# Optimization experiments

Hardware: AMD Instinct MI355X
Metric: run time of the kernel (lower is better)

The kernel has to match this reference:

```python
import jax, jax.numpy as jnp
import numpy as np

B, S, D, H = 4, 2048, 1024, 16
DK = D // H


def setup_inputs() -> dict:
    key = jax.random.key(0)
    ks = jax.random.split(key, 12)
    std = 0.02
    inp = {
        "query": jax.random.normal(ks[0], (B, S, D), jnp.float32),
        "key": jax.random.normal(ks[1], (B, S, D), jnp.float32),
        "value": jax.random.normal(ks[2], (B, S, D), jnp.float32),
        "mask": jnp.ones((B, 1, 1, S), jnp.int32),
        "Wq": jax.random.normal(ks[3], (D, D), jnp.float32) * std,
        "bq": jnp.zeros((D,), jnp.float32),
        "Wk": jax.random.normal(ks[4], (D, D), jnp.float32) * std,
        "bk": jnp.zeros((D,), jnp.float32),
        "Wv": jax.random.normal(ks[5], (D, D), jnp.float32) * std,
        "bv": jnp.zeros((D,), jnp.float32),
        "Wo": jax.random.normal(ks[6], (D, D), jnp.float32) * std,
        "bo": jnp.zeros((D,), jnp.float32),
    }
    return inp


def reference(query, key, value, mask, Wq, bq, Wk, bk, Wv, bv, Wo, bo):
    # nn.Linear: x @ W.T + b; then split heads -> [B, H, S, DK]
    def proj(x, W, b):
        y = x @ W.T + b
        return y.reshape(B, S, H, DK).transpose(0, 2, 1, 3)

    q = proj(query, Wq, bq)
    k = proj(key, Wk, bk)
    v = proj(value, Wv, bv)

    scale = 1.0 / jnp.sqrt(jnp.asarray(DK, q.dtype))
    scores = jnp.einsum('bhqd,bhkd->bhqk', q, k) * scale  # [B,H,S,S]
    scores = jnp.where(mask == 0, jnp.asarray(-1e9, scores.dtype), scores)
    p_attn = jax.nn.softmax(scores, axis=-1)  # dropout p=0 -> identity
    ctx = jnp.einsum('bhqk,bhkd->bhqd', p_attn, v)
    ctx = ctx.transpose(0, 2, 1, 3).reshape(B, S, D)
    out = ctx @ Wo.T + bo
    return out
```

## Files before the change

kernel.cpp:

```cpp
#include <hip/hip_runtime.h>

#define BB 4
#define SS 2048
#define DD 1024
#define HH 16
#define DKC 64
#define MT (BB*SS)
#define NX (MT*DD)
#define NW (DD*DD)

typedef _Float16 f16x8 __attribute__((ext_vector_type(8)));
typedef _Float16 f16x4 __attribute__((ext_vector_type(4)));
typedef float f32x4 __attribute__((ext_vector_type(4)));
typedef int   i32x4 __attribute__((ext_vector_type(4)));

#define GLDS16(g, l)                                                         \
  __builtin_amdgcn_global_load_lds(                                          \
      (__attribute__((address_space(1))) void*)(g),                          \
      (__attribute__((address_space(3))) void*)(l), 16, 0, 0)

__global__ __launch_bounds__(256) void cvt_all(const float* __restrict__ xq,
                                               const float* __restrict__ xk,
                                               const float* __restrict__ xv,
                                               const float* __restrict__ wq,
                                               const float* __restrict__ wk,
                                               const float* __restrict__ wv,
                                               const float* __restrict__ wo,
                                               _Float16* __restrict__ dst) {
  size_t i = ((size_t)blockIdx.x * 256 + threadIdx.x) * 4;
  const float* src; size_t off;
  if (i < (size_t)NX)          { src = xq; off = i; }
  else if (i < (size_t)2*NX)   { src = xk; off = i - (size_t)NX; }
  else if (i < (size_t)3*NX)   { src = xv; off = i - (size_t)2*NX; }
  else {
    size_t j = i - (size_t)3*NX;
    if (j < (size_t)NW)        { src = wq; off = j; }
    else if (j < (size_t)2*NW) { src = wk; off = j - (size_t)NW; }
    else if (j < (size_t)3*NW) { src = wv; off = j - (size_t)2*NW; }
    else                       { src = wo; off = j - (size_t)3*NW; }
  }
  f32x4 f = *(const f32x4*)(src + off);
  f16x4 o;
#pragma unroll
  for (int j = 0; j < 4; ++j) o[j] = (_Float16)f[j];
  *(f16x4*)(dst + i) = o;
}

__global__ __launch_bounds__(256) void gemm_qkv(const _Float16* __restrict__ Xb,
                                                const _Float16* __restrict__ Wb,
                                                const float* __restrict__ b0,
                                                const float* __restrict__ b1,
                                                const float* __restrict__ b2,
                                                _Float16* __restrict__ Pj) {
  const int z = blockIdx.z;
  const _Float16* A = Xb + (size_t)z * MT * DD;
  const _Float16* W = Wb + (size_t)z * DD * DD;
  const float* bias = (z == 0) ? b0 : ((z == 1) ? b1 : b2);
  _Float16* out = Pj + (size_t)z * MT * DD;

  const int m0 = blockIdx.x * 128;
  const int n0 = blockIdx.y * 128;
  const int t = threadIdx.x;
  const int lane = t & 63;
  const int wave = t >> 6;
  const int q = lane >> 4, r = lane & 15;
  const int wm = (wave & 1) * 64, wn = (wave >> 1) * 64;

  __shared__ __align__(16) _Float16 sA[2][128 * 32];
  __shared__ __align__(16) _Float16 sB[2][128 * 32];

  f32x4 acc[4][4] = {};

  const int row0 = t >> 2;
  const int csw = (t & 3) ^ ((t >> 3) & 3);
  const int fsw = (r >> 1) & 3;

  auto stage = [&](int buf, int k0) {
#pragma unroll
    for (int i = 0; i < 2; ++i) {
      GLDS16(A + (size_t)(m0 + row0 + 64 * i) * DD + k0 + csw * 8,
             &sA[buf][(t + 256 * i) * 8]);
      GLDS16(W + (size_t)(n0 + row0 + 64 * i) * DD + k0 + csw * 8,
             &sB[buf][(t + 256 * i) * 8]);
    }
  };

  stage(0, 0);
  __syncthreads();

  int cur = 0;
  for (int k0 = 0; k0 < DD; k0 += 32) {
    if (k0 + 32 < DD) stage(cur ^ 1, k0 + 32);

    f16x8 af[4], bf[4];
#pragma unroll
    for (int x = 0; x < 4; ++x) {
      af[x] = *(const f16x8*)&sA[cur][(wm + x * 16 + r) * 32 + ((q ^ fsw) * 8)];
      bf[x] = *(const f16x8*)&sB[cur][(wn + x * 16 + r) * 32 + ((q ^ fsw) * 8)];
    }
#pragma unroll
    for (int mi = 0; mi < 4; ++mi)
#pragma unroll
      for (int ni = 0; ni < 4; ++ni)
        acc[mi][ni] = __builtin_amdgcn_mfma_f32_16x16x32_f16(af[mi], bf[ni], acc[mi][ni], 0, 0, 0);
    __syncthreads();
    cur ^= 1;
  }

  if (z == 2) {
#pragma unroll
    for (int ni = 0; ni < 4; ++ni) {
      int gn = n0 + wn + ni * 16 + r;
      float bv = bias[gn];
      int h = gn >> 6, dk = gn & 63;
#pragma unroll
      for (int mi = 0; mi < 4; ++mi) {
        int gm = m0 + wm + mi * 16 + q * 4;
        int bb = gm >> 11, s0 = gm & 2047;
        int kl = s0 & 63;
        int kap0 = (kl & 15) * 4 + (kl >> 4);
        size_t base = ((size_t)((bb * HH + h) * DKC + dk)) * SS + (s0 - kl);
#pragma unroll
        for (int rr = 0; rr < 4; ++rr)
          out[base + kap0 + rr * 4] = (_Float16)(acc[mi][ni][rr] + bv);
      }
    }
  } else {
#pragma unroll
    for (int ni = 0; ni < 4; ++ni) {
      int gn = n0 + wn + ni * 16 + r;
      float bv = bias[gn];
      int h = gn >> 6, dk = gn & 63;
#pragma unroll
      for (int mi = 0; mi < 4; ++mi) {
#pragma unroll
        for (int rr = 0; rr < 4; ++rr) {
          int gm = m0 + wm + mi * 16 + q * 4 + rr;
          int bb = gm >> 11, s = gm & 2047;
          out[((size_t)((bb * HH + h) * SS + s)) * DKC + dk] = (_Float16)(acc[mi][ni][rr] + bv);
        }
      }
    }
  }
}

__global__ __launch_bounds__(256) void attn(const _Float16* __restrict__ Pj,
                                            const int* __restrict__ mask,
                                            _Float16* __restrict__ Cx) {
  const int qt = blockIdx.x, h = blockIdx.y, bb = blockIdx.z;
  const size_t hoff = ((size_t)(bb * HH + h) * SS) * DKC;
  const _Float16* Qh  = Pj + hoff;
  const _Float16* Kh  = Pj + (size_t)MT * DD + hoff;
  const _Float16* Vth = Pj + (size_t)2 * MT * DD + hoff;
  _Float16* Ch = Cx + hoff;
  const int* mrow = mask + bb * SS;

  const int t = threadIdx.x, lane = t & 63, wave = t >> 6;
  const int q = lane >> 4, r = lane & 15;
  const int qrow0 = qt * 128 + wave * 32;

  __shared__ __align__(16) _Float16 sK[64 * 64];
  __shared__ __align__(16) _Float16 sVt[64 * 64];
  __shared__ __align__(16) _Float16 sP[4][32 * 64];
  __shared__ __align__(16) _Float16 sMBh[SS];

  {
    int i0 = t * 8;
    i32x4 m0v = *(const i32x4*)(mrow + i0);
    i32x4 m1v = *(const i32x4*)(mrow + i0 + 4);
    f16x8 bvv;
#pragma unroll
    for (int j = 0; j < 4; ++j) {
      bvv[j]     = m0v[j] ? (_Float16)0.0f : (_Float16)(-30000.0f);
      bvv[4 + j] = m1v[j] ? (_Float16)0.0f : (_Float16)(-30000.0f);
    }
    *(f16x8*)&sMBh[i0] = bvv;
  }

  f16x8 qf[2][2];
#pragma unroll
  for (int mi = 0; mi < 2; ++mi)
#pragma unroll
    for (int kk = 0; kk < 2; ++kk)
      qf[mi][kk] = *(const f16x8*)&Qh[(size_t)(qrow0 + mi * 16 + r) * DKC + kk * 32 + q * 8];

  float lst[2][4] = {};
  f32x4 oacc[2][4] = {};

  const float C2 = 0.125f * 1.44269504089f;

  const int srow0 = t >> 3, scc = t & 7;

  f16x8 kpre[2], vpre[2];
#pragma unroll
  for (int i = 0; i < 2; ++i) {
    int row = srow0 + 32 * i;
    kpre[i] = *(const f16x8*)(Kh + (size_t)row * DKC + scc * 8);
    vpre[i] = *(const f16x8*)(Vth + (size_t)row * SS + scc * 8);
  }

  for (int kt = 0; kt < SS; kt += 64) {
#pragma unroll
    for (int i = 0; i < 2; ++i) {
      int row = srow0 + 32 * i;
      *(f16x8*)&sK [row * 64 + ((scc ^ (row & 7)) << 3)] = kpre[i];
      *(f16x8*)&sVt[row * 64 + ((scc ^ (row & 7)) << 3)] = vpre[i];
    }
    __syncthreads();

    if (kt + 64 < SS) {
#pragma unroll
      for (int i = 0; i < 2; ++i) {
        int row = srow0 + 32 * i;
        kpre[i] = *(const f16x8*)(Kh + (size_t)(kt + 64 + row) * DKC + scc * 8);
        vpre[i] = *(const f16x8*)(Vth + (size_t)row * SS + kt + 64 + scc * 8);
      }
    }

    f32x4 sacc[2][4] = {};
#pragma unroll
    for (int kk = 0; kk < 2; ++kk) {
      f16x8 kb[4];
#pragma unroll
      for (int ni = 0; ni < 4; ++ni)
        kb[ni] = *(const f16x8*)&sK[(ni * 16 + r) * 64 + (((kk * 4 + q) ^ (r & 7)) << 3)];
      __builtin_amdgcn_s_setprio(1);
#pragma unroll
      for (int mi = 0; mi < 2; ++mi)
#pragma unroll
        for (int ni = 0; ni < 4; ++ni)
          sacc[mi][ni] = __builtin_amdgcn_mfma_f32_16x16x32_f16(qf[mi][kk], kb[ni], sacc[mi][ni], 0, 0, 0);
      __builtin_amdgcn_s_setprio(0);
    }

    float mb[4];
#pragma unroll
    for (int ni = 0; ni < 4; ++ni) mb[ni] = (float)sMBh[kt + ni * 16 + r];

#pragma unroll
    for (int mi = 0; mi < 2; ++mi) {
#pragma unroll
      for (int rr = 0; rr < 4; ++rr) {
        float pp[4];
#pragma unroll
        for (int ni = 0; ni < 4; ++ni)
          pp[ni] = __builtin_amdgcn_exp2f(__builtin_fmaf(sacc[mi][ni][rr], C2, mb[ni]));
        lst[mi][rr] += (pp[0] + pp[1]) + (pp[2] + pp[3]);
        int prow = mi * 16 + q * 4 + rr;
        int g = (r >> 1) ^ ((q * 4 + rr) & 7);
        int goff = prow * 64 + (g << 3) + ((r & 1) << 2);
        unsigned lo = __builtin_bit_cast(unsigned, __builtin_amdgcn_cvt_pkrtz(pp[0], pp[1]));
        unsigned hi = __builtin_bit_cast(unsigned, __builtin_amdgcn_cvt_pkrtz(pp[2], pp[3]));
        uint2 u; u.x = lo; u.y = hi;
        *(uint2*)&sP[wave][goff] = u;
      }
    }
    __threadfence_block();

#pragma unroll
    for (int kk = 0; kk < 2; ++kk) {
      f16x8 ap[2], vb[4];
#pragma unroll
      for (int mi = 0; mi < 2; ++mi)
        ap[mi] = *(const f16x8*)&sP[wave][(mi * 16 + r) * 64 + (((kk * 4 + q) ^ (r & 7)) << 3)];
#pragma unroll
      for (int ni = 0; ni < 4; ++ni)
        vb[ni] = *(const f16x8*)&sVt[(ni * 16 + r) * 64 + (((kk * 4 + q) ^ (r & 7)) << 3)];
      __builtin_amdgcn_s_setprio(1);
#pragma unroll
      for (int mi = 0; mi < 2; ++mi)
#pragma unroll
        for (int ni = 0; ni < 4; ++ni)
          oacc[mi][ni] = __builtin_amdgcn_mfma_f32_16x16x32_f16(ap[mi], vb[ni], oacc[mi][ni], 0, 0, 0);
      __builtin_amdgcn_s_setprio(0);
    }
    __syncthreads();
  }

#pragma unroll
  for (int mi = 0; mi < 2; ++mi)
#pragma unroll
    for (int rr = 0; rr < 4; ++rr) {
      float l = lst[mi][rr];
#pragma unroll
      for (int d = 1; d < 16; d <<= 1) l += __shfl_xor(l, d);
      lst[mi][rr] = 1.0f / l;
    }

#pragma unroll
  for (int mi = 0; mi < 2; ++mi)
#pragma unroll
    for (int ni = 0; ni < 4; ++ni)
#pragma unroll
      for (int rr = 0; rr < 4; ++rr) {
        int row = qrow0 + mi * 16 + q * 4 + rr;
        Ch[(size_t)row * DKC + ni * 16 + r] = (_Float16)(oacc[mi][ni][rr] * lst[mi][rr]);
      }
}

__global__ __launch_bounds__(256) void gemm_out(const _Float16* __restrict__ Cx,
                                                const _Float16* __restrict__ W,
                                                const float* __restrict__ bias,
                                                float* __restrict__ out) {
  const int m0 = blockIdx.x * 128;
  const int n0 = blockIdx.y * 128;
  const int t = threadIdx.x;
  const int lane = t & 63;
  const int wave = t >> 6;
  const int q = lane >> 4, r = lane & 15;
  const int wm = (wave & 1) * 64, wn = (wave >> 1) * 64;

  __shared__ __align__(16) _Float16 sA[2][128 * 32];
  __shared__ __align__(16) _Float16 sB[2][128 * 32];

  f32x4 acc[4][4] = {};

  const int row0 = t >> 2;
  const int csw = (t & 3) ^ ((t >> 3) & 3);
  const int fsw = (r >> 1) & 3;

  size_t abase[2];
#pragma unroll
  for (int i = 0; i < 2; ++i) {
    int gm = m0 + row0 + 64 * i;
    int bb = gm >> 11, s = gm & 2047;
    abase[i] = ((size_t)(bb * HH) * SS + s) * DKC;
  }

  auto stage = [&](int buf, int k0) {
    int head = k0 >> 6, off = (k0 & 63) + csw * 8;
#pragma unroll
    for (int i = 0; i < 2; ++i) {
      GLDS16(Cx + abase[i] + (size_t)head * SS * DKC + off,
             &sA[buf][(t + 256 * i) * 8]);
      GLDS16(W + (size_t)(n0 + row0 + 64 * i) * DD + k0 + csw * 8,
             &sB[buf][(t + 256 * i) * 8]);
    }
  };

  stage(0, 0);
  __syncthreads();

  int cur = 0;
  for (int k0 = 0; k0 < DD; k0 += 32) {
    if (k0 + 32 < DD) stage(cur ^ 1, k0 + 32);

    f16x8 af[4], bf[4];
#pragma unroll
    for (int x = 0; x < 4; ++x) {
      af[x] = *(const f16x8*)&sA[cur][(wm + x * 16 + r) * 32 + ((q ^ fsw) * 8)];
      bf[x] = *(const f16x8*)&sB[cur][(wn + x * 16 + r) * 32 + ((q ^ fsw) * 8)];
    }
#pragma unroll
    for (int mi = 0; mi < 4; ++mi)
#pragma unroll
      for (int ni = 0; ni < 4; ++ni)
        acc[mi][ni] = __builtin_amdgcn_mfma_f32_16x16x32_f16(af[mi], bf[ni], acc[mi][ni], 0, 0, 0);
    __syncthreads();
    cur ^= 1;
  }

#pragma unroll
  for (int ni = 0; ni < 4; ++ni) {
    int gn = n0 + wn + ni * 16 + r;
    float bv = bias[gn];
#pragma unroll
    for (int mi = 0; mi < 4; ++mi) {
#pragma unroll
      for (int rr = 0; rr < 4; ++rr) {
        int gm = m0 + wm + mi * 16 + q * 4 + rr;
        out[(size_t)gm * DD + gn] = acc[mi][ni][rr] + bv;
      }
    }
  }
}

extern "C" void kernel_launch(void* const* d_in, const int* in_sizes, int n_in,
                              void* d_out, int out_size, void* d_ws, size_t ws_size,
                              hipStream_t stream) {
  const float* query = (const float*)d_in[0];
  const float* key_  = (const float*)d_in[1];
  const float* value = (const float*)d_in[2];
  const int*   mask  = (const int*)d_in[3];
  const float* Wq = (const float*)d_in[4];
  const float* bq = (const float*)d_in[5];
  const float* Wk = (const float*)d_in[6];
  const float* bk = (const float*)d_in[7];
  const float* Wv = (const float*)d_in[8];
  const float* bv = (const float*)d_in[9];
  const float* Wo = (const float*)d_in[10];
  const float* bo = (const float*)d_in[11];
  float* out = (float*)d_out;

  _Float16* Xb = (_Float16*)d_ws;
  _Float16* Wb = Xb + (size_t)3 * NX;
  _Float16* Pj = Wb + (size_t)4 * NW;
  _Float16* Cx = Pj + (size_t)3 * NX;

  cvt_all<<<(3 * NX + 4 * NW) / 1024, 256, 0, stream>>>(query, key_, value, Wq, Wk, Wv, Wo, Xb);

  gemm_qkv<<<dim3(MT / 128, DD / 128, 3), 256, 0, stream>>>(Xb, Wb, bq, bk, bv, Pj);
  attn<<<dim3(SS / 128, HH, BB), 256, 0, stream>>>(Pj, mask, Cx);
  gemm_out<<<dim3(MT / 128, DD / 128), 256, 0, stream>>>(Cx, Wb + (size_t)3 * NW, bo, out);
}
```

Before: 363.6 us.

## Triple-buffer GEMM LDS staging with partial vmcnt waits and single barrier

Both the QKV projection GEMM and the output projection GEMM now use three LDS buffers instead of two. Loads are issued two k-steps ahead, and each step waits only on the older loads with s_waitcnt vmcnt(4) followed by a single barrier, replacing the end-of-loop __syncthreads. The goal is to keep more global loads in flight and remove one barrier per iteration, hiding memory latency behind the MFMA work. This raises LDS use from 32KB to 48KB per block, which may lower occupancy. The hand-written waitcnt counts are also fragile if the compiler reorders the loads.

```diff
diff --git a/kernel.cpp b/kernel.cpp
--- a/kernel.cpp
+++ b/kernel.cpp
@@ -66,8 +66,8 @@
   const int q = lane >> 4, r = lane & 15;
   const int wm = (wave & 1) * 64, wn = (wave >> 1) * 64;
 
-  __shared__ __align__(16) _Float16 sA[2][128 * 32];
-  __shared__ __align__(16) _Float16 sB[2][128 * 32];
+  __shared__ __align__(16) _Float16 sA[3][128 * 32];
+  __shared__ __align__(16) _Float16 sB[3][128 * 32];
 
   f32x4 acc[4][4] = {};
 
@@ -85,27 +85,34 @@
     }
   };
 
-  stage(0, 0);
-  __syncthreads();
-
-  int cur = 0;
-  for (int k0 = 0; k0 < DD; k0 += 32) {
-    if (k0 + 32 < DD) stage(cur ^ 1, k0 + 32);
-
+  auto compute = [&](int buf) {
     f16x8 af[4], bf[4];
 #pragma unroll
     for (int x = 0; x < 4; ++x) {
-      af[x] = *(const f16x8*)&sA[cur][(wm + x * 16 + r) * 32 + ((q ^ fsw) * 8)];
-      bf[x] = *(const f16x8*)&sB[cur][(wn + x * 16 + r) * 32 + ((q ^ fsw) * 8)];
+      af[x] = *(const f16x8*)&sA[buf][(wm + x * 16 + r) * 32 + ((q ^ fsw) * 8)];
+      bf[x] = *(const f16x8*)&sB[buf][(wn + x * 16 + r) * 32 + ((q ^ fsw) * 8)];
     }
 #pragma unroll
     for (int mi = 0; mi < 4; ++mi)
 #pragma unroll
       for (int ni = 0; ni < 4; ++ni)
         acc[mi][ni] = __builtin_amdgcn_mfma_f32_16x16x32_f16(af[mi], bf[ni], acc[mi][ni], 0, 0, 0);
-    __syncthreads();
-    cur ^= 1;
-  }
+  };
+
+  stage(0, 0);
+  stage(1, 32);
+
+  int cur = 0;
+  for (int k0 = 0; k0 < DD - 32; k0 += 32) {
+    asm volatile("s_waitcnt vmcnt(4)" ::: "memory");
+    __builtin_amdgcn_s_barrier();
+    if (k0 + 64 < DD) stage(cur >= 1 ? cur - 1 : cur + 2, k0 + 64);
+    compute(cur);
+    cur = (cur == 2) ? 0 : cur + 1;
+  }
+  asm volatile("s_waitcnt vmcnt(0)" ::: "memory");
+  __builtin_amdgcn_s_barrier();
+  compute(cur);
 
   if (z == 2) {
 #pragma unroll
@@ -310,8 +317,8 @@
   const int q = lane >> 4, r = lane & 15;
   const int wm = (wave & 1) * 64, wn = (wave >> 1) * 64;
 
-  __shared__ __align__(16) _Float16 sA[2][128 * 32];
-  __shared__ __align__(16) _Float16 sB[2][128 * 32];
+  __shared__ __align__(16) _Float16 sA[3][128 * 32];
+  __shared__ __align__(16) _Float16 sB[3][128 * 32];
 
   f32x4 acc[4][4] = {};
 
@@ -338,27 +345,34 @@
     }
   };
 
-  stage(0, 0);
-  __syncthreads();
-
-  int cur = 0;
-  for (int k0 = 0; k0 < DD; k0 += 32) {
-    if (k0 + 32 < DD) stage(cur ^ 1, k0 + 32);
-
+  auto compute = [&](int buf) {
     f16x8 af[4], bf[4];
 #pragma unroll
     for (int x = 0; x < 4; ++x) {
-      af[x] = *(const f16x8*)&sA[cur][(wm + x * 16 + r) * 32 + ((q ^ fsw) * 8)];
-      bf[x] = *(const f16x8*)&sB[cur][(wn + x * 16 + r) * 32 + ((q ^ fsw) * 8)];
+      af[x] = *(const f16x8*)&sA[buf][(wm + x * 16 + r) * 32 + ((q ^ fsw) * 8)];
+      bf[x] = *(const f16x8*)&sB[buf][(wn + x * 16 + r) * 32 + ((q ^ fsw) * 8)];
     }
 #pragma unroll
     for (int mi = 0; mi < 4; ++mi)
 #pragma unroll
       for (int ni = 0; ni < 4; ++ni)
         acc[mi][ni] = __builtin_amdgcn_mfma_f32_16x16x32_f16(af[mi], bf[ni], acc[mi][ni], 0, 0, 0);
-    __syncthreads();
-    cur ^= 1;
-  }
+  };
+
+  stage(0, 0);
+  stage(1, 32);
+
+  int cur = 0;
+  for (int k0 = 0; k0 < DD - 32; k0 += 32) {
+    asm volatile("s_waitcnt vmcnt(4)" ::: "memory");
+    __builtin_amdgcn_s_barrier();
+    if (k0 + 64 < DD) stage(cur >= 1 ? cur - 1 : cur + 2, k0 + 64);
+    compute(cur);
+    cur = (cur == 2) ? 0 : cur + 1;
+  }
+  asm volatile("s_waitcnt vmcnt(0)" ::: "memory");
+  __builtin_amdgcn_s_barrier();
+  compute(cur);
 
 #pragma unroll
   for (int ni = 0; ni < 4; ++ni) {
```

Result: slower. 377.3 us (+3.8%).

## Fuse fp32-to-fp16 conversion into GEMM staging and drop separate convert kernel

Applied to the files above, without the earlier changes.

Removes the standalone conversion kernel that wrote fp16 copies of the inputs and weights. The QKV and output GEMMs now load fp32 tiles into registers, convert them, and store to a single-buffered LDS tile, with a register prefetch of the next tile. This saves one full pass over the activations and weights plus one launch. In exchange, each GEMM reads twice as many input bytes, replaces async global-to-LDS loads with register staging, and goes from double to single LDS buffering, which adds register pressure.

```diff
diff --git a/kernel.cpp b/kernel.cpp
--- a/kernel.cpp
+++ b/kernel.cpp
@@ -14,47 +14,19 @@
 typedef float f32x4 __attribute__((ext_vector_type(4)));
 typedef int   i32x4 __attribute__((ext_vector_type(4)));
 
-#define GLDS16(g, l)                                                         \
-  __builtin_amdgcn_global_load_lds(                                          \
-      (__attribute__((address_space(1))) void*)(g),                          \
-      (__attribute__((address_space(3))) void*)(l), 16, 0, 0)
-
-__global__ __launch_bounds__(256) void cvt_all(const float* __restrict__ xq,
-                                               const float* __restrict__ xk,
-                                               const float* __restrict__ xv,
-                                               const float* __restrict__ wq,
-                                               const float* __restrict__ wk,
-                                               const float* __restrict__ wv,
-                                               const float* __restrict__ wo,
-                                               _Float16* __restrict__ dst) {
-  size_t i = ((size_t)blockIdx.x * 256 + threadIdx.x) * 4;
-  const float* src; size_t off;
-  if (i < (size_t)NX)          { src = xq; off = i; }
-  else if (i < (size_t)2*NX)   { src = xk; off = i - (size_t)NX; }
-  else if (i < (size_t)3*NX)   { src = xv; off = i - (size_t)2*NX; }
-  else {
-    size_t j = i - (size_t)3*NX;
-    if (j < (size_t)NW)        { src = wq; off = j; }
-    else if (j < (size_t)2*NW) { src = wk; off = j - (size_t)NW; }
-    else if (j < (size_t)3*NW) { src = wv; off = j - (size_t)2*NW; }
-    else                       { src = wo; off = j - (size_t)3*NW; }
-  }
-  f32x4 f = *(const f32x4*)(src + off);
-  f16x4 o;
-#pragma unroll
-  for (int j = 0; j < 4; ++j) o[j] = (_Float16)f[j];
-  *(f16x4*)(dst + i) = o;
-}
-
-__global__ __launch_bounds__(256) void gemm_qkv(const _Float16* __restrict__ Xb,
-                                                const _Float16* __restrict__ Wb,
+__global__ __launch_bounds__(256) void gemm_qkv(const float* __restrict__ xq,
+                                                const float* __restrict__ xk,
+                                                const float* __restrict__ xv,
+                                                const float* __restrict__ wq,
+                                                const float* __restrict__ wk,
+                                                const float* __restrict__ wv,
                                                 const float* __restrict__ b0,
                                                 const float* __restrict__ b1,
                                                 const float* __restrict__ b2,
                                                 _Float16* __restrict__ Pj) {
   const int z = blockIdx.z;
-  const _Float16* A = Xb + (size_t)z * MT * DD;
-  const _Float16* W = Wb + (size_t)z * DD * DD;
+  const float* A = (z == 0) ? xq : ((z == 1) ? xk : xv);
+  const float* W = (z == 0) ? wq : ((z == 1) ? wk : wv);
   const float* bias = (z == 0) ? b0 : ((z == 1) ? b1 : b2);
   _Float16* out = Pj + (size_t)z * MT * DD;
 
@@ -66,37 +38,56 @@
   const int q = lane >> 4, r = lane & 15;
   const int wm = (wave & 1) * 64, wn = (wave >> 1) * 64;
 
-  __shared__ __align__(16) _Float16 sA[2][128 * 32];
-  __shared__ __align__(16) _Float16 sB[2][128 * 32];
+  __shared__ __align__(16) _Float16 sA[128 * 32];
+  __shared__ __align__(16) _Float16 sB[128 * 32];
 
   f32x4 acc[4][4] = {};
 
-  const int row0 = t >> 2;
-  const int csw = (t & 3) ^ ((t >> 3) & 3);
+  const int row0 = t >> 2, cc = t & 3;
+  const int wch = (t & 3) ^ ((t >> 3) & 3);
   const int fsw = (r >> 1) & 3;
 
-  auto stage = [&](int buf, int k0) {
+  f32x4 apre[2][2], bpre[2][2];
+
+  auto prefetch = [&](int k0) {
 #pragma unroll
     for (int i = 0; i < 2; ++i) {
-      GLDS16(A + (size_t)(m0 + row0 + 64 * i) * DD + k0 + csw * 8,
-             &sA[buf][(t + 256 * i) * 8]);
-      GLDS16(W + (size_t)(n0 + row0 + 64 * i) * DD + k0 + csw * 8,
-             &sB[buf][(t + 256 * i) * 8]);
+      const float* pa = A + (size_t)(m0 + row0 + 64 * i) * DD + k0 + cc * 8;
+      const float* pb = W + (size_t)(n0 + row0 + 64 * i) * DD + k0 + cc * 8;
+      apre[i][0] = *(const f32x4*)pa;  apre[i][1] = *(const f32x4*)(pa + 4);
+      bpre[i][0] = *(const f32x4*)pb;  bpre[i][1] = *(const f32x4*)(pb + 4);
     }
   };
 
-  stage(0, 0);
-  __syncthreads();
-
-  int cur = 0;
+  auto commit = [&]() {
+#pragma unroll
+    for (int i = 0; i < 2; ++i) {
+      int row = row0 + 64 * i;
+      f16x8 av, bv8;
+#pragma unroll
+      for (int j = 0; j < 4; ++j) {
+        av[j]      = (_Float16)apre[i][0][j];
+        av[4 + j]  = (_Float16)apre[i][1][j];
+        bv8[j]     = (_Float16)bpre[i][0][j];
+        bv8[4 + j] = (_Float16)bpre[i][1][j];
+      }
+      *(f16x8*)&sA[row * 32 + wch * 8] = av;
+      *(f16x8*)&sB[row * 32 + wch * 8] = bv8;
+    }
+  };
+
+  prefetch(0);
+
   for (int k0 = 0; k0 < DD; k0 += 32) {
-    if (k0 + 32 < DD) stage(cur ^ 1, k0 + 32);
+    commit();
+    __syncthreads();
+    if (k0 + 32 < DD) prefetch(k0 + 32);
 
     f16x8 af[4], bf[4];
 #pragma unroll
     for (int x = 0; x < 4; ++x) {
-      af[x] = *(const f16x8*)&sA[cur][(wm + x * 16 + r) * 32 + ((q ^ fsw) * 8)];
-      bf[x] = *(const f16x8*)&sB[cur][(wn + x * 16 + r) * 32 + ((q ^ fsw) * 8)];
+      af[x] = *(const f16x8*)&sA[(wm + x * 16 + r) * 32 + ((q ^ fsw) * 8)];
+      bf[x] = *(const f16x8*)&sB[(wn + x * 16 + r) * 32 + ((q ^ fsw) * 8)];
     }
 #pragma unroll
     for (int mi = 0; mi < 4; ++mi)
@@ -104,7 +95,6 @@
       for (int ni = 0; ni < 4; ++ni)
         acc[mi][ni] = __builtin_amdgcn_mfma_f32_16x16x32_f16(af[mi], bf[ni], acc[mi][ni], 0, 0, 0);
     __syncthreads();
-    cur ^= 1;
   }
 
   if (z == 2) {
@@ -299,7 +289,7 @@
 }
 
 __global__ __launch_bounds__(256) void gemm_out(const _Float16* __restrict__ Cx,
-                                                const _Float16* __restrict__ W,
+                                                const float* __restrict__ W,
                                                 const float* __restrict__ bias,
                                                 float* __restrict__ out) {
   const int m0 = blockIdx.x * 128;
@@ -310,13 +300,13 @@
   const int q = lane >> 4, r = lane & 15;
   const int wm = (wave & 1) * 64, wn = (wave >> 1) * 64;
 
-  __shared__ __align__(16) _Float16 sA[2][128 * 32];
-  __shared__ __align__(16) _Float16 sB[2][128 * 32];
+  __shared__ __align__(16) _Float16 sA[128 * 32];
+  __shared__ __align__(16) _Float16 sB[128 * 32];
 
   f32x4 acc[4][4] = {};
 
-  const int row0 = t >> 2;
-  const int csw = (t & 3) ^ ((t >> 3) & 3);
+  const int row0 = t >> 2, cc = t & 3;
+  const int wch = (t & 3) ^ ((t >> 3) & 3);
   const int fsw = (r >> 1) & 3;
 
   size_t abase[2];
@@ -327,29 +317,46 @@
     abase[i] = ((size_t)(bb * HH) * SS + s) * DKC;
   }
 
-  auto stage = [&](int buf, int k0) {
-    int head = k0 >> 6, off = (k0 & 63) + csw * 8;
+  f16x8 apre[2];
+  f32x4 bpre[2][2];
+
+  auto prefetch = [&](int k0) {
+    int head = k0 >> 6, off = (k0 & 63) + cc * 8;
 #pragma unroll
     for (int i = 0; i < 2; ++i) {
-      GLDS16(Cx + abase[i] + (size_t)head * SS * DKC + off,
-             &sA[buf][(t + 256 * i) * 8]);
-      GLDS16(W + (size_t)(n0 + row0 + 64 * i) * DD + k0 + csw * 8,
-             &sB[buf][(t + 256 * i) * 8]);
+      apre[i] = *(const f16x8*)(Cx + abase[i] + (size_t)head * SS * DKC + off);
+      const float* pb = W + (size_t)(n0 + row0 + 64 * i) * DD + k0 + cc * 8;
+      bpre[i][0] = *(const f32x4*)pb;  bpre[i][1] = *(const f32x4*)(pb + 4);
     }
   };
 
-  stage(0, 0);
-  __syncthreads();
-
-  int cur = 0;
+  auto commit = [&]() {
+#pragma unroll
+    for (int i = 0; i < 2; ++i) {
+      int row = row0 + 64 * i;
+      f16x8 bv8;
+#pragma unroll
+      for (int j = 0; j < 4; ++j) {
+        bv8[j]     = (_Float16)bpre[i][0][j];
+        bv8[4 + j] = (_Float16)bpre[i][1][j];
+      }
+      *(f16x8*)&sA[row * 32 + wch * 8] = apre[i];
+      *(f16x8*)&sB[row * 32 + wch * 8] = bv8;
+    }
+  };
+
+  prefetch(0);
+
   for (int k0 = 0; k0 < DD; k0 += 32) {
-    if (k0 + 32 < DD) stage(cur ^ 1, k0 + 32);
+    commit();
+    __syncthreads();
+    if (k0 + 32 < DD) prefetch(k0 + 32);
 
     f16x8 af[4], bf[4];
 #pragma unroll
     for (int x = 0; x < 4; ++x) {
-      af[x] = *(const f16x8*)&sA[cur][(wm + x * 16 + r) * 32 + ((q ^ fsw) * 8)];
-      bf[x] = *(const f16x8*)&sB[cur][(wn + x * 16 + r) * 32 + ((q ^ fsw) * 8)];
+      af[x] = *(const f16x8*)&sA[(wm + x * 16 + r) * 32 + ((q ^ fsw) * 8)];
+      bf[x] = *(const f16x8*)&sB[(wn + x * 16 + r) * 32 + ((q ^ fsw) * 8)];
     }
 #pragma unroll
     for (int mi = 0; mi < 4; ++mi)
@@ -357,7 +364,6 @@
       for (int ni = 0; ni < 4; ++ni)
         acc[mi][ni] = __builtin_amdgcn_mfma_f32_16x16x32_f16(af[mi], bf[ni], acc[mi][ni], 0, 0, 0);
     __syncthreads();
-    cur ^= 1;
   }
 
 #pragma unroll
@@ -392,14 +398,11 @@
   const float* bo = (const float*)d_in[11];
   float* out = (float*)d_out;
 
-  _Float16* Xb = (_Float16*)d_ws;
-  _Float16* Wb = Xb + (size_t)3 * NX;
-  _Float16* Pj = Wb + (size_t)4 * NW;
+  _Float16* Pj = (_Float16*)d_ws;
   _Float16* Cx = Pj + (size_t)3 * NX;
 
-  cvt_all<<<(3 * NX + 4 * NW) / 1024, 256, 0, stream>>>(query, key_, value, Wq, Wk, Wv, Wo, Xb);
-
-  gemm_qkv<<<dim3(MT / 128, DD / 128, 3), 256, 0, stream>>>(Xb, Wb, bq, bk, bv, Pj);
+  gemm_qkv<<<dim3(MT / 128, DD / 128, 3), 256, 0, stream>>>(query, key_, value, Wq, Wk, Wv,
+                                                            bq, bk, bv, Pj);
   attn<<<dim3(SS / 128, HH, BB), 256, 0, stream>>>(Pj, mask, Cx);
-  gemm_out<<<dim3(MT / 128, DD / 128), 256, 0, stream>>>(Cx, Wb + (size_t)3 * NW, bo, out);
+  gemm_out<<<dim3(MT / 128, DD / 128), 256, 0, stream>>>(Cx, Wo, bo, out);
 }
```

Result: slower. 399.4 us (+9.8%).

## Shrink GEMM tiles to 64x128 and stage through registers instead of direct-to-LDS loads

Applied to the files above, without the earlier changes.

Both projection GEMMs switch from 128x128 tiles with double-buffered global_load_lds staging to 64x128 tiles. Each tile is loaded into registers, prefetched one k-step ahead, and written to a single LDS buffer. This halves per-block LDS and accumulator registers and doubles the block count, aiming for better occupancy and load balance. The cost is lower data reuse per block and an extra register-to-LDS round trip with two barriers per k-step.

```diff
diff --git a/kernel.cpp b/kernel.cpp
--- a/kernel.cpp
+++ b/kernel.cpp
@@ -13,11 +13,6 @@
 typedef _Float16 f16x4 __attribute__((ext_vector_type(4)));
 typedef float f32x4 __attribute__((ext_vector_type(4)));
 typedef int   i32x4 __attribute__((ext_vector_type(4)));
-
-#define GLDS16(g, l)                                                         \
-  __builtin_amdgcn_global_load_lds(                                          \
-      (__attribute__((address_space(1))) void*)(g),                          \
-      (__attribute__((address_space(3))) void*)(l), 16, 0, 0)
 
 __global__ __launch_bounds__(256) void cvt_all(const float* __restrict__ xq,
                                                const float* __restrict__ xk,
@@ -58,53 +53,59 @@
   const float* bias = (z == 0) ? b0 : ((z == 1) ? b1 : b2);
   _Float16* out = Pj + (size_t)z * MT * DD;
 
-  const int m0 = blockIdx.x * 128;
+  const int m0 = blockIdx.x * 64;
   const int n0 = blockIdx.y * 128;
   const int t = threadIdx.x;
   const int lane = t & 63;
   const int wave = t >> 6;
   const int q = lane >> 4, r = lane & 15;
-  const int wm = (wave & 1) * 64, wn = (wave >> 1) * 64;
-
-  __shared__ __align__(16) _Float16 sA[2][128 * 32];
-  __shared__ __align__(16) _Float16 sB[2][128 * 32];
-
-  f32x4 acc[4][4] = {};
-
-  const int row0 = t >> 2;
-  const int csw = (t & 3) ^ ((t >> 3) & 3);
+  const int wm = (wave & 1) * 32, wn = (wave >> 1) * 64;
+
+  __shared__ __align__(16) _Float16 sA[64 * 32];
+  __shared__ __align__(16) _Float16 sB[128 * 32];
+
+  f32x4 acc[2][4] = {};
+
+  const int row0 = t >> 2, cc = t & 3;
+  const int wch = (t & 3) ^ ((t >> 3) & 3);
   const int fsw = (r >> 1) & 3;
 
-  auto stage = [&](int buf, int k0) {
-#pragma unroll
-    for (int i = 0; i < 2; ++i) {
-      GLDS16(A + (size_t)(m0 + row0 + 64 * i) * DD + k0 + csw * 8,
-             &sA[buf][(t + 256 * i) * 8]);
-      GLDS16(W + (size_t)(n0 + row0 + 64 * i) * DD + k0 + csw * 8,
-             &sB[buf][(t + 256 * i) * 8]);
-    }
+  f16x8 apre, bpre[2];
+
+  auto prefetch = [&](int k0) {
+    apre = *(const f16x8*)(A + (size_t)(m0 + row0) * DD + k0 + cc * 8);
+#pragma unroll
+    for (int i = 0; i < 2; ++i)
+      bpre[i] = *(const f16x8*)(W + (size_t)(n0 + row0 + 64 * i) * DD + k0 + cc * 8);
   };
 
-  stage(0, 0);
-  __syncthreads();
-
-  int cur = 0;
+  auto commit = [&]() {
+    *(f16x8*)&sA[row0 * 32 + wch * 8] = apre;
+#pragma unroll
+    for (int i = 0; i < 2; ++i)
+      *(f16x8*)&sB[(row0 + 64 * i) * 32 + wch * 8] = bpre[i];
+  };
+
+  prefetch(0);
+
   for (int k0 = 0; k0 < DD; k0 += 32) {
-    if (k0 + 32 < DD) stage(cur ^ 1, k0 + 32);
-
-    f16x8 af[4], bf[4];
-#pragma unroll
-    for (int x = 0; x < 4; ++x) {
-      af[x] = *(const f16x8*)&sA[cur][(wm + x * 16 + r) * 32 + ((q ^ fsw) * 8)];
-      bf[x] = *(const f16x8*)&sB[cur][(wn + x * 16 + r) * 32 + ((q ^ fsw) * 8)];
-    }
-#pragma unroll
-    for (int mi = 0; mi < 4; ++mi)
+    commit();
+    __syncthreads();
+    if (k0 + 32 < DD) prefetch(k0 + 32);
+
+    f16x8 af[2], bf[4];
+#pragma unroll
+    for (int mi = 0; mi < 2; ++mi)
+      af[mi] = *(const f16x8*)&sA[(wm + mi * 16 + r) * 32 + ((q ^ fsw) * 8)];
+#pragma unroll
+    for (int ni = 0; ni < 4; ++ni)
+      bf[ni] = *(const f16x8*)&sB[(wn + ni * 16 + r) * 32 + ((q ^ fsw) * 8)];
+#pragma unroll
+    for (int mi = 0; mi < 2; ++mi)
 #pragma unroll
       for (int ni = 0; ni < 4; ++ni)
         acc[mi][ni] = __builtin_amdgcn_mfma_f32_16x16x32_f16(af[mi], bf[ni], acc[mi][ni], 0, 0, 0);
     __syncthreads();
-    cur ^= 1;
   }
 
   if (z == 2) {
@@ -114,7 +115,7 @@
       float bv = bias[gn];
       int h = gn >> 6, dk = gn & 63;
 #pragma unroll
-      for (int mi = 0; mi < 4; ++mi) {
+      for (int mi = 0; mi < 2; ++mi) {
         int gm = m0 + wm + mi * 16 + q * 4;
         int bb = gm >> 11, s0 = gm & 2047;
         int kl = s0 & 63;
@@ -132,7 +133,7 @@
       float bv = bias[gn];
       int h = gn >> 6, dk = gn & 63;
 #pragma unroll
-      for (int mi = 0; mi < 4; ++mi) {
+      for (int mi = 0; mi < 2; ++mi) {
 #pragma unroll
         for (int rr = 0; rr < 4; ++rr) {
           int gm = m0 + wm + mi * 16 + q * 4 + rr;
@@ -302,62 +303,67 @@
                                                 const _Float16* __restrict__ W,
                                                 const float* __restrict__ bias,
                                                 float* __restrict__ out) {
-  const int m0 = blockIdx.x * 128;
+  const int m0 = blockIdx.x * 64;
   const int n0 = blockIdx.y * 128;
   const int t = threadIdx.x;
   const int lane = t & 63;
   const int wave = t >> 6;
   const int q = lane >> 4, r = lane & 15;
-  const int wm = (wave & 1) * 64, wn = (wave >> 1) * 64;
-
-  __shared__ __align__(16) _Float16 sA[2][128 * 32];
-  __shared__ __align__(16) _Float16 sB[2][128 * 32];
-
-  f32x4 acc[4][4] = {};
-
-  const int row0 = t >> 2;
-  const int csw = (t & 3) ^ ((t >> 3) & 3);
+  const int wm = (wave & 1) * 32, wn = (wave >> 1) * 64;
+
+  __shared__ __align__(16) _Float16 sA[64 * 32];
+  __shared__ __align__(16) _Float16 sB[128 * 32];
+
+  f32x4 acc[2][4] = {};
+
+  const int row0 = t >> 2, cc = t & 3;
+  const int wch = (t & 3) ^ ((t >> 3) & 3);
   const int fsw = (r >> 1) & 3;
 
-  size_t abase[2];
-#pragma unroll
-  for (int i = 0; i < 2; ++i) {
-    int gm = m0 + row0 + 64 * i;
+  size_t abase;
+  {
+    int gm = m0 + row0;
     int bb = gm >> 11, s = gm & 2047;
-    abase[i] = ((size_t)(bb * HH) * SS + s) * DKC;
-  }
-
-  auto stage = [&](int buf, int k0) {
-    int head = k0 >> 6, off = (k0 & 63) + csw * 8;
-#pragma unroll
-    for (int i = 0; i < 2; ++i) {
-      GLDS16(Cx + abase[i] + (size_t)head * SS * DKC + off,
-             &sA[buf][(t + 256 * i) * 8]);
-      GLDS16(W + (size_t)(n0 + row0 + 64 * i) * DD + k0 + csw * 8,
-             &sB[buf][(t + 256 * i) * 8]);
-    }
+    abase = ((size_t)(bb * HH) * SS + s) * DKC;
+  }
+
+  f16x8 apre, bpre[2];
+
+  auto prefetch = [&](int k0) {
+    int head = k0 >> 6, off = (k0 & 63) + cc * 8;
+    apre = *(const f16x8*)(Cx + abase + (size_t)head * SS * DKC + off);
+#pragma unroll
+    for (int i = 0; i < 2; ++i)
+      bpre[i] = *(const f16x8*)(W + (size_t)(n0 + row0 + 64 * i) * DD + k0 + cc * 8);
   };
 
-  stage(0, 0);
-  __syncthreads();
-
-  int cur = 0;
+  auto commit = [&]() {
+    *(f16x8*)&sA[row0 * 32 + wch * 8] = apre;
+#pragma unroll
+    for (int i = 0; i < 2; ++i)
+      *(f16x8*)&sB[(row0 + 64 * i) * 32 + wch * 8] = bpre[i];
+  };
+
+  prefetch(0);
+
   for (int k0 = 0; k0 < DD; k0 += 32) {
-    if (k0 + 32 < DD) stage(cur ^ 1, k0 + 32);
-
-    f16x8 af[4], bf[4];
-#pragma unroll
-    for (int x = 0; x < 4; ++x) {
-      af[x] = *(const f16x8*)&sA[cur][(wm + x * 16 + r) * 32 + ((q ^ fsw) * 8)];
-      bf[x] = *(const f16x8*)&sB[cur][(wn + x * 16 + r) * 32 + ((q ^ fsw) * 8)];
-    }
-#pragma unroll
-    for (int mi = 0; mi < 4; ++mi)
+    commit();
+    __syncthreads();
+    if (k0 + 32 < DD) prefetch(k0 + 32);
+
+    f16x8 af[2], bf[4];
+#pragma unroll
+    for (int mi = 0; mi < 2; ++mi)
+      af[mi] = *(const f16x8*)&sA[(wm + mi * 16 + r) * 32 + ((q ^ fsw) * 8)];
+#pragma unroll
+    for (int ni = 0; ni < 4; ++ni)
+      bf[ni] = *(const f16x8*)&sB[(wn + ni * 16 + r) * 32 + ((q ^ fsw) * 8)];
+#pragma unroll
+    for (int mi = 0; mi < 2; ++mi)
 #pragma unroll
       for (int ni = 0; ni < 4; ++ni)
         acc[mi][ni] = __builtin_amdgcn_mfma_f32_16x16x32_f16(af[mi], bf[ni], acc[mi][ni], 0, 0, 0);
     __syncthreads();
-    cur ^= 1;
   }
 
 #pragma unroll
@@ -365,7 +371,7 @@
     int gn = n0 + wn + ni * 16 + r;
     float bv = bias[gn];
 #pragma unroll
-    for (int mi = 0; mi < 4; ++mi) {
+    for (int mi = 0; mi < 2; ++mi) {
 #pragma unroll
       for (int rr = 0; rr < 4; ++rr) {
         int gm = m0 + wm + mi * 16 + q * 4 + rr;
@@ -399,7 +405,7 @@
 
   cvt_all<<<(3 * NX + 4 * NW) / 1024, 256, 0, stream>>>(query, key_, value, Wq, Wk, Wv, Wo, Xb);
 
-  gemm_qkv<<<dim3(MT / 128, DD / 128, 3), 256, 0, stream>>>(Xb, Wb, bq, bk, bv, Pj);
+  gemm_qkv<<<dim3(MT / 64, DD / 128, 3), 256, 0, stream>>>(Xb, Wb, bq, bk, bv, Pj);
   attn<<<dim3(SS / 128, HH, BB), 256, 0, stream>>>(Pj, mask, Cx);
-  gemm_out<<<dim3(MT / 128, DD / 128), 256, 0, stream>>>(Cx, Wb + (size_t)3 * NW, bo, out);
+  gemm_out<<<dim3(MT / 64, DD / 128), 256, 0, stream>>>(Cx, Wb + (size_t)3 * NW, bo, out);
 }
```

Result: slower. 385.6 us (+6.0%).
